# Kernel optimization log

Hardware: AMD Instinct MI355X
Metric: run time of the kernel (lower is better)

Reference implementation:

```python
import jax, jax.numpy as jnp
import numpy as np

H = 1024
S = 2048
B = 16

def setup_inputs() -> dict:
    key = jax.random.key(0)
    k1, k2, k3, k4, k5, k6 = jax.random.split(key, 6)
    hidden = jax.random.normal(k1, (1, B, H), dtype=jnp.float32)
    encoder_outputs = jax.random.normal(k2, (S, B, H), dtype=jnp.float32)
    seq_mask = jax.random.randint(k3, (B, S), 0, 2, dtype=jnp.int32)
    # nn.Linear(2H, H): weight [H, 2H], bias [H]
    lim1 = 1.0 / np.sqrt(2 * H)
    attn_w = jax.random.uniform(k4, (H, 2 * H), minval=-lim1, maxval=lim1, dtype=jnp.float32)
    attn_b = jax.random.uniform(k5, (H,), minval=-lim1, maxval=lim1, dtype=jnp.float32)
    # nn.Linear(H, 1, bias=False): weight [1, H]
    lim2 = 1.0 / np.sqrt(H)
    score_w = jax.random.uniform(k6, (1, H), minval=-lim2, maxval=lim2, dtype=jnp.float32)
    return {"hidden": hidden, "encoder_outputs": encoder_outputs, "seq_mask": seq_mask,
            "attn_w": attn_w, "attn_b": attn_b, "score_w": score_w}

def reference(hidden, encoder_outputs, seq_mask, attn_w, attn_b, score_w):
    # Faithful to: cat([hidden.repeat(S,1,1), encoder_outputs], -1) @ attn_w.T + attn_b
    # Split the concat-linear into two GEMMs (identical math, avoids the big concat).
    h = hidden.shape[-1]
    Wh = attn_w[:, :h]   # acts on repeated hidden
    We = attn_w[:, h:]   # acts on encoder outputs
    # hidden: [1,B,H] broadcasts over S; encoder_outputs: [S,B,H]
    pre = jnp.einsum('obh,kh->obk', hidden, Wh) + jnp.einsum('sbh,kh->sbk', encoder_outputs, We) + attn_b
    proj = jnp.tanh(pre)                               # [S,B,H]
    energies = jnp.einsum('sbh,oh->sbo', proj, score_w)[..., 0]  # [S,B]
    energies = energies.T                              # [B,S] (transpose(0,1) in original)
    energies = jnp.where(seq_mask.astype(bool), jnp.float32(-1e12), energies)
    attn = jax.nn.softmax(energies, axis=1)            # [B,S]
    return attn[:, None, :]                            # [B,1,S]
```

## Files before the change

### kernel.cpp

```cpp
#include <hip/hip_runtime.h>
#include <hip/hip_bf16.h>

#define HDIM 1024
#define SEQ 2048
#define BATCH 16
#define M_TOT (SEQ*BATCH)
#define NBLK 4
#define BM 256
#define BN 256
#define BKT 64
#define NT (HDIM/BKT)

typedef __attribute__((ext_vector_type(8))) short short8;
typedef __attribute__((ext_vector_type(4))) float f32x4;

typedef const void __attribute__((address_space(1))) gvoid_t;
typedef void __attribute__((address_space(3))) svoid_t;
#define GLD16(gp, lp) __builtin_amdgcn_global_load_lds((gvoid_t*)(gp), (svoid_t*)(lp), 16, 0, 0)
#define VMC(N) asm volatile("s_waitcnt vmcnt(" #N ")" ::: "memory")

static __device__ __forceinline__ unsigned short f2bf(float f) {
    unsigned int x = __float_as_uint(f);
    unsigned int r = (x + 0x7FFFu + ((x >> 16) & 1u)) >> 16;
    return (unsigned short)r;
}

__global__ __launch_bounds__(256) void qk_kernel(const float* __restrict__ hidden,
                                                 const float* __restrict__ attn_w,
                                                 const float* __restrict__ attn_b,
                                                 float* __restrict__ q) {
    int k = blockIdx.x;
    int tid = threadIdx.x;
    const float* w = attn_w + (size_t)k * (2 * HDIM);
    float p[BATCH];
#pragma unroll
    for (int b = 0; b < BATCH; b++) p[b] = 0.f;
    for (int h = tid; h < HDIM; h += 256) {
        float wv = w[h];
#pragma unroll
        for (int b = 0; b < BATCH; b++) p[b] += hidden[b * HDIM + h] * wv;
    }
#pragma unroll
    for (int b = 0; b < BATCH; b++) {
        for (int off = 32; off; off >>= 1) p[b] += __shfl_down(p[b], off);
    }
    __shared__ float red[4][BATCH];
    int lane = tid & 63, wid = tid >> 6;
    if (lane == 0) {
#pragma unroll
        for (int b = 0; b < BATCH; b++) red[wid][b] = p[b];
    }
    __syncthreads();
    if (tid < BATCH) {
        float s = red[0][tid] + red[1][tid] + red[2][tid] + red[3][tid] + attn_b[k];
        q[(size_t)tid * HDIM + k] = s;
    }
}

__global__ __launch_bounds__(256) void conv_kernel(const float* __restrict__ attn_w,
                                                   __hip_bfloat16* __restrict__ web) {
    size_t i0 = ((size_t)blockIdx.x * 256 + threadIdx.x) * 8;
    int n = (int)(i0 >> 10);
    int h = (int)(i0 & 1023);
    const float4* src = reinterpret_cast<const float4*>(attn_w + (size_t)n * (2 * HDIM) + HDIM + h);
    float4 a = src[0], b = src[1];
    union { unsigned short u[8]; short8 v; } cv;
    cv.u[0] = f2bf(a.x); cv.u[1] = f2bf(a.y); cv.u[2] = f2bf(a.z); cv.u[3] = f2bf(a.w);
    cv.u[4] = f2bf(b.x); cv.u[5] = f2bf(b.y); cv.u[6] = f2bf(b.z); cv.u[7] = f2bf(b.w);
    *reinterpret_cast<short8*>((unsigned short*)web + i0) = cv.v;
}

__global__ __launch_bounds__(256) void conv_enc(const float* __restrict__ src,
                                                __hip_bfloat16* __restrict__ dst) {
    size_t i0 = ((size_t)blockIdx.x * 256 + threadIdx.x) * 8;
    const float4* s = reinterpret_cast<const float4*>(src + i0);
    float4 a = s[0], b = s[1];
    union { unsigned short u[8]; short8 v; } cv;
    cv.u[0] = f2bf(a.x); cv.u[1] = f2bf(a.y); cv.u[2] = f2bf(a.z); cv.u[3] = f2bf(a.w);
    cv.u[4] = f2bf(b.x); cv.u[5] = f2bf(b.y); cv.u[6] = f2bf(b.z); cv.u[7] = f2bf(b.w);
    *reinterpret_cast<short8*>((unsigned short*)dst + i0) = cv.v;
}

__global__ __launch_bounds__(512, 2) void gemm8(const __hip_bfloat16* __restrict__ encb,
                                                const __hip_bfloat16* __restrict__ web,
                                                const float* __restrict__ qv,
                                                const float* __restrict__ score_w,
                                                float* __restrict__ part) {
    __shared__ __align__(16) char pool[131072];

    int tid = threadIdx.x;
    int lane = tid & 63;
    int wid = tid >> 6;
    int wr = wid >> 2;
    int wc = wid & 3;

    int bid = blockIdx.x;
    int lin = (bid & 7) * 64 + (bid >> 3);
    int bm = lin >> 2;
    int bn = lin & 3;
    int m0 = bm * BM, n0 = bn * BN;

    int srow = tid >> 3;
    int scolb = (((tid & 7) ^ ((tid >> 3) & 7)) << 4);
    const char* eb = (const char*)encb;
    const char* wb = (const char*)web;

    auto STG = [&](const char* g, int ldsoff) {
        GLD16(g + (size_t)srow * 2048 + scolb, pool + ldsoff + wid * 1024);
        GLD16(g + (size_t)(srow + 64) * 2048 + scolb, pool + ldsoff + 8192 + wid * 1024);
    };
    auto APTR = [&](int kt, int h) { return eb + ((size_t)(m0 + h * 128) * HDIM + kt * BKT) * 2; };
    auto BPTR = [&](int kt, int h) { return wb + ((size_t)(n0 + h * 128) * HDIM + kt * BKT) * 2; };
#define ALDS(par, h) ((par) * 32768 + (h) * 16384)
#define BLDS(par, h) (65536 + (par) * 32768 + (h) * 16384)

    int lq = lane & 15, lh = lane >> 4;
    int flip = (lane & 7) << 4;
    int pks0 = lq * 128 + ((lh * 16) ^ flip);
    int pks1 = lq * 128 + (((64 + lh * 16)) ^ flip);
    int aFB = wr * 16384;
    int bFB = 65536 + (wc >> 1) * 16384 + (wc & 1) * 8192;

    f32x4 acc[8][4];
#pragma unroll
    for (int i = 0; i < 8; i++)
#pragma unroll
        for (int j = 0; j < 4; j++) acc[i][j] = (f32x4)0.f;
    short8 br[4][2];

#define RD8(off) (*reinterpret_cast<const short8*>(pool + (off)))

#define PHASE(Q, PAR, STAGE_STMT, PRE_CLOSE)                                              \
    {                                                                                     \
        if ((Q) == 0) {                                                                   \
            _Pragma("unroll") for (int nj = 0; nj < 4; ++nj) {                            \
                br[nj][0] = RD8(bFB + (PAR) * 32768 + nj * 2048 + pks0);                  \
                br[nj][1] = RD8(bFB + (PAR) * 32768 + nj * 2048 + pks1);                  \
            }                                                                             \
        }                                                                                 \
        short8 a0k0 = RD8(aFB + (PAR) * 32768 + (2 * (Q)) * 2048 + pks0);                 \
        short8 a0k1 = RD8(aFB + (PAR) * 32768 + (2 * (Q)) * 2048 + pks1);                 \
        short8 a1k0 = RD8(aFB + (PAR) * 32768 + (2 * (Q) + 1) * 2048 + pks0);             \
        short8 a1k1 = RD8(aFB + (PAR) * 32768 + (2 * (Q) + 1) * 2048 + pks1);             \
        STAGE_STMT;                                                                       \
        __builtin_amdgcn_s_barrier();                                                     \
        __builtin_amdgcn_s_setprio(1);                                                    \
        _Pragma("unroll") for (int nj = 0; nj < 4; ++nj) {                                \
            acc[2 * (Q)][nj] = __builtin_amdgcn_mfma_f32_16x16x32_bf16(a0k0, br[nj][0], acc[2 * (Q)][nj], 0, 0, 0); \
            acc[2 * (Q)][nj] = __builtin_amdgcn_mfma_f32_16x16x32_bf16(a0k1, br[nj][1], acc[2 * (Q)][nj], 0, 0, 0); \
            acc[2 * (Q) + 1][nj] = __builtin_amdgcn_mfma_f32_16x16x32_bf16(a1k0, br[nj][0], acc[2 * (Q) + 1][nj], 0, 0, 0); \
            acc[2 * (Q) + 1][nj] = __builtin_amdgcn_mfma_f32_16x16x32_bf16(a1k1, br[nj][1], acc[2 * (Q) + 1][nj], 0, 0, 0); \
        }                                                                                 \
        __builtin_amdgcn_s_setprio(0);                                                    \
        PRE_CLOSE;                                                                        \
        __builtin_amdgcn_s_barrier();                                                     \
        __builtin_amdgcn_sched_barrier(0);                                                \
    }

    STG(BPTR(0, 0), BLDS(0, 0));
    STG(BPTR(0, 1), BLDS(0, 1));
    STG(APTR(0, 0), ALDS(0, 0));
    STG(APTR(0, 1), ALDS(0, 1));
    STG(BPTR(1, 0), BLDS(1, 0));
    STG(BPTR(1, 1), BLDS(1, 1));
    VMC(4);
    __builtin_amdgcn_s_barrier();
    __builtin_amdgcn_sched_barrier(0);

#pragma unroll 1
    for (int J = 0; J < 7; ++J) {
        int k1 = 2 * J + 1;
        PHASE(0, 0, STG(APTR(k1, 0), ALDS(1, 0)), );
        PHASE(1, 0, STG(APTR(k1, 1), ALDS(1, 1)), );
        PHASE(2, 0, STG(BPTR(k1 + 1, 0), BLDS(0, 0)), );
        PHASE(3, 0, STG(BPTR(k1 + 1, 1), BLDS(0, 1)), VMC(4));
        PHASE(0, 1, STG(APTR(k1 + 1, 0), ALDS(0, 0)), );
        PHASE(1, 1, STG(APTR(k1 + 1, 1), ALDS(0, 1)), );
        PHASE(2, 1, STG(BPTR(k1 + 2, 0), BLDS(1, 0)), );
        PHASE(3, 1, STG(BPTR(k1 + 2, 1), BLDS(1, 1)), VMC(4));
    }
    PHASE(0, 0, STG(APTR(15, 0), ALDS(1, 0)), );
    PHASE(1, 0, STG(APTR(15, 1), ALDS(1, 1)), );
    PHASE(2, 0, , );
    PHASE(3, 0, , VMC(0));
    PHASE(0, 1, , );
    PHASE(1, 1, , );
    PHASE(2, 1, , );
    PHASE(3, 1, , );

    float* q_lds = reinterpret_cast<float*>(pool);
    float* sc_lds = reinterpret_cast<float*>(pool + 16384);
    float* eng = reinterpret_cast<float*>(pool + 17408);
    {
        int qb = tid >> 5;
        int kl = (tid & 31) * 8;
        const float4* src = reinterpret_cast<const float4*>(qv + (size_t)qb * HDIM + n0 + kl);
        float4 v0 = src[0], v1 = src[1];
        *reinterpret_cast<float4*>(&q_lds[qb * 256 + kl]) = v0;
        *reinterpret_cast<float4*>(&q_lds[qb * 256 + kl + 4]) = v1;
        if (tid < BN) sc_lds[tid] = score_w[n0 + tid];
    }
    __syncthreads();

#pragma unroll
    for (int mi = 0; mi < 8; ++mi) {
#pragma unroll
        for (int r = 0; r < 4; ++r) {
            int b = lh * 4 + r;
            float s = 0.f;
#pragma unroll
            for (int nj = 0; nj < 4; ++nj) {
                int kl = wc * 64 + nj * 16 + lq;
                float v = acc[mi][nj][r] + q_lds[b * 256 + kl];
                float t = 1.f - 2.f / (__expf(2.f * v) + 1.f);
                s += sc_lds[kl] * t;
            }
            for (int off = 1; off < 16; off <<= 1) s += __shfl_xor(s, off);
            if (lq == 0) eng[wc * 256 + wr * 128 + mi * 16 + b] = s;
        }
    }
    __syncthreads();
    if (tid < BM) {
        float s = eng[tid] + eng[256 + tid] + eng[512 + tid] + eng[768 + tid];
        part[(size_t)bn * M_TOT + m0 + tid] = s;
    }
#undef PHASE
#undef RD8
#undef ALDS
#undef BLDS
}

__global__ __launch_bounds__(256) void softmax_kernel(const float* __restrict__ part,
                                                      const int* __restrict__ mask,
                                                      float* __restrict__ out) {
    int b = blockIdx.x;
    int tid = threadIdx.x;
    __shared__ float e_lds[SEQ];
    __shared__ float red[4], red2[4];
    int lane = tid & 63, wid = tid >> 6;
    float lmax = -3.4e38f;
    for (int it = 0; it < SEQ / 256; ++it) {
        int s = it * 256 + tid;
        size_t m = (size_t)s * BATCH + b;
        float e = 0.f;
#pragma unroll
        for (int c = 0; c < NBLK; c++) e += part[(size_t)c * M_TOT + m];
        if (mask[(size_t)b * SEQ + s]) e = -1e12f;
        e_lds[s] = e;
        lmax = fmaxf(lmax, e);
    }
    for (int off = 32; off; off >>= 1) lmax = fmaxf(lmax, __shfl_xor(lmax, off));
    if (lane == 0) red[wid] = lmax;
    __syncthreads();
    float gmax = fmaxf(fmaxf(red[0], red[1]), fmaxf(red[2], red[3]));
    float lsum = 0.f;
    for (int it = 0; it < SEQ / 256; ++it) {
        int s = it * 256 + tid;
        float p = __expf(e_lds[s] - gmax);
        e_lds[s] = p;
        lsum += p;
    }
    for (int off = 32; off; off >>= 1) lsum += __shfl_xor(lsum, off);
    if (lane == 0) red2[wid] = lsum;
    __syncthreads();
    float inv = 1.f / (red2[0] + red2[1] + red2[2] + red2[3]);
    for (int it = 0; it < SEQ / 256; ++it) {
        int s = it * 256 + tid;
        out[(size_t)b * SEQ + s] = e_lds[s] * inv;
    }
}

extern "C" void kernel_launch(void* const* d_in, const int* in_sizes, int n_in,
                              void* d_out, int out_size, void* d_ws, size_t ws_size,
                              hipStream_t stream) {
    const float* hidden   = (const float*)d_in[0];
    const float* enc      = (const float*)d_in[1];
    const int*   seq_mask = (const int*)d_in[2];
    const float* attn_w   = (const float*)d_in[3];
    const float* attn_b   = (const float*)d_in[4];
    const float* score_w  = (const float*)d_in[5];
    float* out = (float*)d_out;

    char* ws = (char*)d_ws;
    float* q = (float*)ws;
    __hip_bfloat16* web = (__hip_bfloat16*)(ws + 65536);
    float* part = (float*)(ws + 65536 + 2 * 1024 * 1024);
    __hip_bfloat16* encb = (__hip_bfloat16*)(ws + 65536 + 3 * 1024 * 1024);

    conv_enc<<<dim3((M_TOT * HDIM) / (8 * 256)), dim3(256), 0, stream>>>(enc, encb);
    conv_kernel<<<dim3((HDIM * HDIM) / (8 * 256)), dim3(256), 0, stream>>>(attn_w, web);
    qk_kernel<<<dim3(HDIM), dim3(256), 0, stream>>>(hidden, attn_w, attn_b, q);
    gemm8<<<dim3(NBLK * (M_TOT / BM)), dim3(512), 0, stream>>>(encb, web, q, score_w, part);
    softmax_kernel<<<dim3(BATCH), dim3(256), 0, stream>>>(part, seq_mask, out);
}
```

Before: 121.7 us.

## Fuse fp32-to-bf16 encoder conversion into GEMM A-tile loads via registers

```diff
diff --git a/kernel.cpp b/kernel.cpp
--- a/kernel.cpp
+++ b/kernel.cpp
@@ -18,6 +18,7 @@
 typedef void __attribute__((address_space(3))) svoid_t;
 #define GLD16(gp, lp) __builtin_amdgcn_global_load_lds((gvoid_t*)(gp), (svoid_t*)(lp), 16, 0, 0)
 #define VMC(N) asm volatile("s_waitcnt vmcnt(" #N ")" ::: "memory")
+#define LGKM0 asm volatile("s_waitcnt lgkmcnt(0)" ::: "memory")
 
 static __device__ __forceinline__ unsigned short f2bf(float f) {
     unsigned int x = __float_as_uint(f);
@@ -70,18 +71,7 @@
     *reinterpret_cast<short8*>((unsigned short*)web + i0) = cv.v;
 }
 
-__global__ __launch_bounds__(256) void conv_enc(const float* __restrict__ src,
-                                                __hip_bfloat16* __restrict__ dst) {
-    size_t i0 = ((size_t)blockIdx.x * 256 + threadIdx.x) * 8;
-    const float4* s = reinterpret_cast<const float4*>(src + i0);
-    float4 a = s[0], b = s[1];
-    union { unsigned short u[8]; short8 v; } cv;
-    cv.u[0] = f2bf(a.x); cv.u[1] = f2bf(a.y); cv.u[2] = f2bf(a.z); cv.u[3] = f2bf(a.w);
-    cv.u[4] = f2bf(b.x); cv.u[5] = f2bf(b.y); cv.u[6] = f2bf(b.z); cv.u[7] = f2bf(b.w);
-    *reinterpret_cast<short8*>((unsigned short*)dst + i0) = cv.v;
-}
-
-__global__ __launch_bounds__(512, 2) void gemm8(const __hip_bfloat16* __restrict__ encb,
+__global__ __launch_bounds__(512, 2) void gemm8(const float* __restrict__ enc,
                                                 const __hip_bfloat16* __restrict__ web,
                                                 const float* __restrict__ qv,
                                                 const float* __restrict__ score_w,
@@ -102,17 +92,43 @@
 
     int srow = tid >> 3;
     int scolb = (((tid & 7) ^ ((tid >> 3) & 7)) << 4);
-    const char* eb = (const char*)encb;
     const char* wb = (const char*)web;
 
     auto STG = [&](const char* g, int ldsoff) {
         GLD16(g + (size_t)srow * 2048 + scolb, pool + ldsoff + wid * 1024);
         GLD16(g + (size_t)(srow + 64) * 2048 + scolb, pool + ldsoff + 8192 + wid * 1024);
     };
-    auto APTR = [&](int kt, int h) { return eb + ((size_t)(m0 + h * 128) * HDIM + kt * BKT) * 2; };
     auto BPTR = [&](int kt, int h) { return wb + ((size_t)(n0 + h * 128) * HDIM + kt * BKT) * 2; };
 #define ALDS(par, h) ((par) * 32768 + (h) * 16384)
 #define BLDS(par, h) (65536 + (par) * 32768 + (h) * 16384)
+
+    int ar = tid >> 2;
+    int ac = (tid & 3) * 16;
+    int awc = ((tid & 3) * 32) ^ ((ar & 7) << 4);
+    float4 av_e[8], av_o[8];
+
+    auto ALD = [&](float4* d, int kt, int h) {
+        const float4* p = reinterpret_cast<const float4*>(enc + (size_t)(m0 + h * 128 + ar) * HDIM + kt * BKT + ac);
+        d[0] = p[0]; d[1] = p[1]; d[2] = p[2]; d[3] = p[3];
+    };
+    auto AWR = [&](float4* v, int par) {
+#pragma unroll
+        for (int h = 0; h < 2; ++h) {
+            const float4* s4 = v + h * 4;
+            union { __hip_bfloat162 b[4]; short8 s; } w0, w1;
+            w0.b[0] = __float22bfloat162_rn(make_float2(s4[0].x, s4[0].y));
+            w0.b[1] = __float22bfloat162_rn(make_float2(s4[0].z, s4[0].w));
+            w0.b[2] = __float22bfloat162_rn(make_float2(s4[1].x, s4[1].y));
+            w0.b[3] = __float22bfloat162_rn(make_float2(s4[1].z, s4[1].w));
+            w1.b[0] = __float22bfloat162_rn(make_float2(s4[2].x, s4[2].y));
+            w1.b[1] = __float22bfloat162_rn(make_float2(s4[2].z, s4[2].w));
+            w1.b[2] = __float22bfloat162_rn(make_float2(s4[3].x, s4[3].y));
+            w1.b[3] = __float22bfloat162_rn(make_float2(s4[3].z, s4[3].w));
+            char* base = pool + par * 32768 + h * 16384 + ar * 128;
+            *reinterpret_cast<short8*>(base + awc) = w0.s;
+            *reinterpret_cast<short8*>(base + (awc ^ 16)) = w1.s;
+        }
+    };
 
     int lq = lane & 15, lh = lane >> 4;
     int flip = (lane & 7) << 4;
@@ -157,32 +173,37 @@
         __builtin_amdgcn_sched_barrier(0);                                                \
     }
 
+    ALD(av_o, 0, 0);
+    ALD(av_o + 4, 0, 1);
     STG(BPTR(0, 0), BLDS(0, 0));
     STG(BPTR(0, 1), BLDS(0, 1));
-    STG(APTR(0, 0), ALDS(0, 0));
-    STG(APTR(0, 1), ALDS(0, 1));
+    VMC(4);
+    AWR(av_o, 0);
+    ALD(av_o, 1, 0);
+    ALD(av_o + 4, 1, 1);
     STG(BPTR(1, 0), BLDS(1, 0));
     STG(BPTR(1, 1), BLDS(1, 1));
-    VMC(4);
+    VMC(12);
+    LGKM0;
     __builtin_amdgcn_s_barrier();
     __builtin_amdgcn_sched_barrier(0);
 
 #pragma unroll 1
     for (int J = 0; J < 7; ++J) {
-        int k1 = 2 * J + 1;
-        PHASE(0, 0, STG(APTR(k1, 0), ALDS(1, 0)), );
-        PHASE(1, 0, STG(APTR(k1, 1), ALDS(1, 1)), );
-        PHASE(2, 0, STG(BPTR(k1 + 1, 0), BLDS(0, 0)), );
-        PHASE(3, 0, STG(BPTR(k1 + 1, 1), BLDS(0, 1)), VMC(4));
-        PHASE(0, 1, STG(APTR(k1 + 1, 0), ALDS(0, 0)), );
-        PHASE(1, 1, STG(APTR(k1 + 1, 1), ALDS(0, 1)), );
-        PHASE(2, 1, STG(BPTR(k1 + 2, 0), BLDS(1, 0)), );
-        PHASE(3, 1, STG(BPTR(k1 + 2, 1), BLDS(1, 1)), VMC(4));
-    }
-    PHASE(0, 0, STG(APTR(15, 0), ALDS(1, 0)), );
-    PHASE(1, 0, STG(APTR(15, 1), ALDS(1, 1)), );
-    PHASE(2, 0, , );
-    PHASE(3, 0, , VMC(0));
+        int ke = 2 * J + 2, ko = 2 * J + 3;
+        PHASE(0, 0, ALD(av_e, ke, 0), );
+        PHASE(1, 0, ALD(av_e + 4, ke, 1), );
+        PHASE(2, 0, { VMC(8); AWR(av_o, 1); }, LGKM0);
+        PHASE(3, 0, { STG(BPTR(ke, 0), BLDS(0, 0)); STG(BPTR(ke, 1), BLDS(0, 1)); }, );
+        PHASE(0, 1, ALD(av_o, ko, 0), );
+        PHASE(1, 1, ALD(av_o + 4, ko, 1), );
+        PHASE(2, 1, { VMC(8); AWR(av_e, 0); }, LGKM0);
+        PHASE(3, 1, { STG(BPTR(ko, 0), BLDS(1, 0)); STG(BPTR(ko, 1), BLDS(1, 1)); }, );
+    }
+    PHASE(0, 0, , );
+    PHASE(1, 0, , );
+    PHASE(2, 0, { VMC(0); AWR(av_o, 1); }, LGKM0);
+    PHASE(3, 0, , );
     PHASE(0, 1, , );
     PHASE(1, 1, , );
     PHASE(2, 1, , );
@@ -285,11 +306,9 @@
     float* q = (float*)ws;
     __hip_bfloat16* web = (__hip_bfloat16*)(ws + 65536);
     float* part = (float*)(ws + 65536 + 2 * 1024 * 1024);
-    __hip_bfloat16* encb = (__hip_bfloat16*)(ws + 65536 + 3 * 1024 * 1024);
-
-    conv_enc<<<dim3((M_TOT * HDIM) / (8 * 256)), dim3(256), 0, stream>>>(enc, encb);
+
     conv_kernel<<<dim3((HDIM * HDIM) / (8 * 256)), dim3(256), 0, stream>>>(attn_w, web);
     qk_kernel<<<dim3(HDIM), dim3(256), 0, stream>>>(hidden, attn_w, attn_b, q);
-    gemm8<<<dim3(NBLK * (M_TOT / BM)), dim3(512), 0, stream>>>(encb, web, q, score_w, part);
+    gemm8<<<dim3(NBLK * (M_TOT / BM)), dim3(512), 0, stream>>>(enc, web, q, score_w, part);
     softmax_kernel<<<dim3(BATCH), dim3(256), 0, stream>>>(part, seq_mask, out);
 }
```

Result: slower. 226.8 us (+86.4%).

## Fuse encoder fp32-to-bf16 conversion into GEMM A-tile loads and merge prep kernels

Applied to the files above, without the earlier changes.

```diff
diff --git a/kernel.cpp b/kernel.cpp
--- a/kernel.cpp
+++ b/kernel.cpp
@@ -5,9 +5,9 @@
 #define SEQ 2048
 #define BATCH 16
 #define M_TOT (SEQ*BATCH)
-#define NBLK 4
+#define NBLK 8
 #define BM 256
-#define BN 256
+#define BN 128
 #define BKT 64
 #define NT (HDIM/BKT)
 
@@ -18,6 +18,7 @@
 typedef void __attribute__((address_space(3))) svoid_t;
 #define GLD16(gp, lp) __builtin_amdgcn_global_load_lds((gvoid_t*)(gp), (svoid_t*)(lp), 16, 0, 0)
 #define VMC(N) asm volatile("s_waitcnt vmcnt(" #N ")" ::: "memory")
+#define LGKM0 asm volatile("s_waitcnt lgkmcnt(0)" ::: "memory")
 
 static __device__ __forceinline__ unsigned short f2bf(float f) {
     unsigned int x = __float_as_uint(f);
@@ -25,11 +26,25 @@
     return (unsigned short)r;
 }
 
-__global__ __launch_bounds__(256) void qk_kernel(const float* __restrict__ hidden,
-                                                 const float* __restrict__ attn_w,
-                                                 const float* __restrict__ attn_b,
-                                                 float* __restrict__ q) {
-    int k = blockIdx.x;
+__global__ __launch_bounds__(256) void prep_kernel(const float* __restrict__ hidden,
+                                                   const float* __restrict__ attn_w,
+                                                   const float* __restrict__ attn_b,
+                                                   float* __restrict__ q,
+                                                   __hip_bfloat16* __restrict__ web) {
+    int bid = blockIdx.x;
+    if (bid < 512) {
+        size_t i0 = ((size_t)bid * 256 + threadIdx.x) * 8;
+        int n = (int)(i0 >> 10);
+        int h = (int)(i0 & 1023);
+        const float4* src = reinterpret_cast<const float4*>(attn_w + (size_t)n * (2 * HDIM) + HDIM + h);
+        float4 a = src[0], b = src[1];
+        union { unsigned short u[8]; short8 v; } cv;
+        cv.u[0] = f2bf(a.x); cv.u[1] = f2bf(a.y); cv.u[2] = f2bf(a.z); cv.u[3] = f2bf(a.w);
+        cv.u[4] = f2bf(b.x); cv.u[5] = f2bf(b.y); cv.u[6] = f2bf(b.z); cv.u[7] = f2bf(b.w);
+        *reinterpret_cast<short8*>((unsigned short*)web + i0) = cv.v;
+        return;
+    }
+    int k = bid - 512;
     int tid = threadIdx.x;
     const float* w = attn_w + (size_t)k * (2 * HDIM);
     float p[BATCH];
@@ -57,153 +72,154 @@
     }
 }
 
-__global__ __launch_bounds__(256) void conv_kernel(const float* __restrict__ attn_w,
-                                                   __hip_bfloat16* __restrict__ web) {
-    size_t i0 = ((size_t)blockIdx.x * 256 + threadIdx.x) * 8;
-    int n = (int)(i0 >> 10);
-    int h = (int)(i0 & 1023);
-    const float4* src = reinterpret_cast<const float4*>(attn_w + (size_t)n * (2 * HDIM) + HDIM + h);
-    float4 a = src[0], b = src[1];
-    union { unsigned short u[8]; short8 v; } cv;
-    cv.u[0] = f2bf(a.x); cv.u[1] = f2bf(a.y); cv.u[2] = f2bf(a.z); cv.u[3] = f2bf(a.w);
-    cv.u[4] = f2bf(b.x); cv.u[5] = f2bf(b.y); cv.u[6] = f2bf(b.z); cv.u[7] = f2bf(b.w);
-    *reinterpret_cast<short8*>((unsigned short*)web + i0) = cv.v;
-}
-
-__global__ __launch_bounds__(256) void conv_enc(const float* __restrict__ src,
-                                                __hip_bfloat16* __restrict__ dst) {
-    size_t i0 = ((size_t)blockIdx.x * 256 + threadIdx.x) * 8;
-    const float4* s = reinterpret_cast<const float4*>(src + i0);
-    float4 a = s[0], b = s[1];
-    union { unsigned short u[8]; short8 v; } cv;
-    cv.u[0] = f2bf(a.x); cv.u[1] = f2bf(a.y); cv.u[2] = f2bf(a.z); cv.u[3] = f2bf(a.w);
-    cv.u[4] = f2bf(b.x); cv.u[5] = f2bf(b.y); cv.u[6] = f2bf(b.z); cv.u[7] = f2bf(b.w);
-    *reinterpret_cast<short8*>((unsigned short*)dst + i0) = cv.v;
-}
-
-__global__ __launch_bounds__(512, 2) void gemm8(const __hip_bfloat16* __restrict__ encb,
+__global__ __launch_bounds__(512, 2) void gemm8(const float* __restrict__ enc,
                                                 const __hip_bfloat16* __restrict__ web,
                                                 const float* __restrict__ qv,
                                                 const float* __restrict__ score_w,
                                                 float* __restrict__ part) {
-    __shared__ __align__(16) char pool[131072];
+    __shared__ __align__(16) char pool[98304];
 
     int tid = threadIdx.x;
     int lane = tid & 63;
     int wid = tid >> 6;
-    int wr = wid >> 2;
-    int wc = wid & 3;
+    int wr = wid >> 1;
+    int wc = wid & 1;
 
     int bid = blockIdx.x;
-    int lin = (bid & 7) * 64 + (bid >> 3);
-    int bm = lin >> 2;
-    int bn = lin & 3;
+    int lin = (bid & 7) * 128 + (bid >> 3);
+    int bm = lin >> 3;
+    int bn = lin & 7;
     int m0 = bm * BM, n0 = bn * BN;
 
-    int srow = tid >> 3;
-    int scolb = (((tid & 7) ^ ((tid >> 3) & 7)) << 4);
-    const char* eb = (const char*)encb;
     const char* wb = (const char*)web;
-
-    auto STG = [&](const char* g, int ldsoff) {
-        GLD16(g + (size_t)srow * 2048 + scolb, pool + ldsoff + wid * 1024);
-        GLD16(g + (size_t)(srow + 64) * 2048 + scolb, pool + ldsoff + 8192 + wid * 1024);
+    int brow = wid * 8 + (lane >> 3);
+    int bsegb = (((lane & 7) ^ ((lane >> 3) & 7)) << 4);
+    auto BSTG = [&](int kt, int p) {
+        const char* g0 = wb + ((size_t)(n0 + brow) * HDIM + kt * BKT) * 2 + bsegb;
+        GLD16(g0, pool + 65536 + p * 16384 + wid * 1024);
+        const char* g1 = wb + ((size_t)(n0 + 64 + brow) * HDIM + kt * BKT) * 2 + bsegb;
+        GLD16(g1, pool + 65536 + p * 16384 + 8192 + wid * 1024);
     };
-    auto APTR = [&](int kt, int h) { return eb + ((size_t)(m0 + h * 128) * HDIM + kt * BKT) * 2; };
-    auto BPTR = [&](int kt, int h) { return wb + ((size_t)(n0 + h * 128) * HDIM + kt * BKT) * 2; };
-#define ALDS(par, h) ((par) * 32768 + (h) * 16384)
-#define BLDS(par, h) (65536 + (par) * 32768 + (h) * 16384)
+
+    int arow = tid >> 1;
+    int ah = tid & 1;
+    const float* abase = enc + (size_t)(m0 + arow) * HDIM + ah * 32;
+    float4 av[8];
+    auto ALD = [&](int kt) {
+        const float4* p = reinterpret_cast<const float4*>(abase + kt * BKT);
+#pragma unroll
+        for (int i = 0; i < 8; i++) av[i] = p[i];
+    };
+    int ar7 = arow & 7;
+    auto AWR = [&](int p) {
+        char* base = pool + p * 32768 + arow * 128;
+#pragma unroll
+        for (int w = 0; w < 4; w++) {
+            union { __hip_bfloat162 b[4]; short8 s; } u;
+            u.b[0] = __float22bfloat162_rn(make_float2(av[2 * w].x, av[2 * w].y));
+            u.b[1] = __float22bfloat162_rn(make_float2(av[2 * w].z, av[2 * w].w));
+            u.b[2] = __float22bfloat162_rn(make_float2(av[2 * w + 1].x, av[2 * w + 1].y));
+            u.b[3] = __float22bfloat162_rn(make_float2(av[2 * w + 1].z, av[2 * w + 1].w));
+            *reinterpret_cast<short8*>(base + (((ah * 4 + w) ^ ar7) << 4)) = u.s;
+        }
+    };
 
     int lq = lane & 15, lh = lane >> 4;
-    int flip = (lane & 7) << 4;
-    int pks0 = lq * 128 + ((lh * 16) ^ flip);
-    int pks1 = lq * 128 + (((64 + lh * 16)) ^ flip);
-    int aFB = wr * 16384;
-    int bFB = 65536 + (wc >> 1) * 16384 + (wc & 1) * 8192;
-
-    f32x4 acc[8][4];
-#pragma unroll
-    for (int i = 0; i < 8; i++)
+    int s0 = ((lh ^ (lq & 7)) << 4);
+    int s1 = (((4 + lh) ^ (lq & 7)) << 4);
+    int aRB = (wr * 64 + lq) * 128;
+    int bRB = 65536 + (wc * 64 + lq) * 128;
+
+    f32x4 acc[4][4];
+#pragma unroll
+    for (int i = 0; i < 4; i++)
 #pragma unroll
         for (int j = 0; j < 4; j++) acc[i][j] = (f32x4)0.f;
     short8 br[4][2];
 
 #define RD8(off) (*reinterpret_cast<const short8*>(pool + (off)))
 
-#define PHASE(Q, PAR, STAGE_STMT, PRE_CLOSE)                                              \
+#define PH1(PAR, T)                                                                       \
     {                                                                                     \
-        if ((Q) == 0) {                                                                   \
-            _Pragma("unroll") for (int nj = 0; nj < 4; ++nj) {                            \
-                br[nj][0] = RD8(bFB + (PAR) * 32768 + nj * 2048 + pks0);                  \
-                br[nj][1] = RD8(bFB + (PAR) * 32768 + nj * 2048 + pks1);                  \
-            }                                                                             \
+        _Pragma("unroll") for (int nj = 0; nj < 4; ++nj) {                                \
+            br[nj][0] = RD8(bRB + (PAR) * 16384 + nj * 2048 + s0);                        \
+            br[nj][1] = RD8(bRB + (PAR) * 16384 + nj * 2048 + s1);                        \
         }                                                                                 \
-        short8 a0k0 = RD8(aFB + (PAR) * 32768 + (2 * (Q)) * 2048 + pks0);                 \
-        short8 a0k1 = RD8(aFB + (PAR) * 32768 + (2 * (Q)) * 2048 + pks1);                 \
-        short8 a1k0 = RD8(aFB + (PAR) * 32768 + (2 * (Q) + 1) * 2048 + pks0);             \
-        short8 a1k1 = RD8(aFB + (PAR) * 32768 + (2 * (Q) + 1) * 2048 + pks1);             \
-        STAGE_STMT;                                                                       \
+        short8 a00 = RD8(aRB + (PAR) * 32768 + 0 * 2048 + s0);                            \
+        short8 a01 = RD8(aRB + (PAR) * 32768 + 0 * 2048 + s1);                            \
+        short8 a10 = RD8(aRB + (PAR) * 32768 + 1 * 2048 + s0);                            \
+        short8 a11 = RD8(aRB + (PAR) * 32768 + 1 * 2048 + s1);                            \
+        if ((T) < 15) ALD((T) + 1);                                                       \
         __builtin_amdgcn_s_barrier();                                                     \
         __builtin_amdgcn_s_setprio(1);                                                    \
         _Pragma("unroll") for (int nj = 0; nj < 4; ++nj) {                                \
-            acc[2 * (Q)][nj] = __builtin_amdgcn_mfma_f32_16x16x32_bf16(a0k0, br[nj][0], acc[2 * (Q)][nj], 0, 0, 0); \
-            acc[2 * (Q)][nj] = __builtin_amdgcn_mfma_f32_16x16x32_bf16(a0k1, br[nj][1], acc[2 * (Q)][nj], 0, 0, 0); \
-            acc[2 * (Q) + 1][nj] = __builtin_amdgcn_mfma_f32_16x16x32_bf16(a1k0, br[nj][0], acc[2 * (Q) + 1][nj], 0, 0, 0); \
-            acc[2 * (Q) + 1][nj] = __builtin_amdgcn_mfma_f32_16x16x32_bf16(a1k1, br[nj][1], acc[2 * (Q) + 1][nj], 0, 0, 0); \
+            acc[0][nj] = __builtin_amdgcn_mfma_f32_16x16x32_bf16(a00, br[nj][0], acc[0][nj], 0, 0, 0); \
+            acc[0][nj] = __builtin_amdgcn_mfma_f32_16x16x32_bf16(a01, br[nj][1], acc[0][nj], 0, 0, 0); \
+            acc[1][nj] = __builtin_amdgcn_mfma_f32_16x16x32_bf16(a10, br[nj][0], acc[1][nj], 0, 0, 0); \
+            acc[1][nj] = __builtin_amdgcn_mfma_f32_16x16x32_bf16(a11, br[nj][1], acc[1][nj], 0, 0, 0); \
         }                                                                                 \
         __builtin_amdgcn_s_setprio(0);                                                    \
-        PRE_CLOSE;                                                                        \
         __builtin_amdgcn_s_barrier();                                                     \
         __builtin_amdgcn_sched_barrier(0);                                                \
     }
 
-    STG(BPTR(0, 0), BLDS(0, 0));
-    STG(BPTR(0, 1), BLDS(0, 1));
-    STG(APTR(0, 0), ALDS(0, 0));
-    STG(APTR(0, 1), ALDS(0, 1));
-    STG(BPTR(1, 0), BLDS(1, 0));
-    STG(BPTR(1, 1), BLDS(1, 1));
-    VMC(4);
+#define PH2(PAR, T)                                                                       \
+    {                                                                                     \
+        short8 a00 = RD8(aRB + (PAR) * 32768 + 2 * 2048 + s0);                            \
+        short8 a01 = RD8(aRB + (PAR) * 32768 + 2 * 2048 + s1);                            \
+        short8 a10 = RD8(aRB + (PAR) * 32768 + 3 * 2048 + s0);                            \
+        short8 a11 = RD8(aRB + (PAR) * 32768 + 3 * 2048 + s1);                            \
+        VMC(0);                                                                           \
+        if ((T) < 15) AWR((PAR) ^ 1);                                                     \
+        if ((T) < 14) BSTG((T) + 2, (PAR));                                               \
+        LGKM0;                                                                            \
+        __builtin_amdgcn_sched_barrier(0);                                                \
+        __builtin_amdgcn_s_barrier();                                                     \
+        __builtin_amdgcn_s_setprio(1);                                                    \
+        _Pragma("unroll") for (int nj = 0; nj < 4; ++nj) {                                \
+            acc[2][nj] = __builtin_amdgcn_mfma_f32_16x16x32_bf16(a00, br[nj][0], acc[2][nj], 0, 0, 0); \
+            acc[2][nj] = __builtin_amdgcn_mfma_f32_16x16x32_bf16(a01, br[nj][1], acc[2][nj], 0, 0, 0); \
+            acc[3][nj] = __builtin_amdgcn_mfma_f32_16x16x32_bf16(a10, br[nj][0], acc[3][nj], 0, 0, 0); \
+            acc[3][nj] = __builtin_amdgcn_mfma_f32_16x16x32_bf16(a11, br[nj][1], acc[3][nj], 0, 0, 0); \
+        }                                                                                 \
+        __builtin_amdgcn_s_setprio(0);                                                    \
+        __builtin_amdgcn_s_barrier();                                                     \
+        __builtin_amdgcn_sched_barrier(0);                                                \
+    }
+
+    ALD(0);
+    VMC(0);
+    AWR(0);
+    BSTG(0, 0);
+    BSTG(1, 1);
+    VMC(2);
+    LGKM0;
     __builtin_amdgcn_s_barrier();
     __builtin_amdgcn_sched_barrier(0);
 
 #pragma unroll 1
-    for (int J = 0; J < 7; ++J) {
-        int k1 = 2 * J + 1;
-        PHASE(0, 0, STG(APTR(k1, 0), ALDS(1, 0)), );
-        PHASE(1, 0, STG(APTR(k1, 1), ALDS(1, 1)), );
-        PHASE(2, 0, STG(BPTR(k1 + 1, 0), BLDS(0, 0)), );
-        PHASE(3, 0, STG(BPTR(k1 + 1, 1), BLDS(0, 1)), VMC(4));
-        PHASE(0, 1, STG(APTR(k1 + 1, 0), ALDS(0, 0)), );
-        PHASE(1, 1, STG(APTR(k1 + 1, 1), ALDS(0, 1)), );
-        PHASE(2, 1, STG(BPTR(k1 + 2, 0), BLDS(1, 0)), );
-        PHASE(3, 1, STG(BPTR(k1 + 2, 1), BLDS(1, 1)), VMC(4));
-    }
-    PHASE(0, 0, STG(APTR(15, 0), ALDS(1, 0)), );
-    PHASE(1, 0, STG(APTR(15, 1), ALDS(1, 1)), );
-    PHASE(2, 0, , );
-    PHASE(3, 0, , VMC(0));
-    PHASE(0, 1, , );
-    PHASE(1, 1, , );
-    PHASE(2, 1, , );
-    PHASE(3, 1, , );
+    for (int tp = 0; tp < 8; ++tp) {
+        int t0 = 2 * tp, t1 = 2 * tp + 1;
+        PH1(0, t0);
+        PH2(0, t0);
+        PH1(1, t1);
+        PH2(1, t1);
+    }
 
     float* q_lds = reinterpret_cast<float*>(pool);
-    float* sc_lds = reinterpret_cast<float*>(pool + 16384);
-    float* eng = reinterpret_cast<float*>(pool + 17408);
+    float* sc_lds = reinterpret_cast<float*>(pool + 8192);
+    float* eng = reinterpret_cast<float*>(pool + 8704);
     {
         int qb = tid >> 5;
-        int kl = (tid & 31) * 8;
-        const float4* src = reinterpret_cast<const float4*>(qv + (size_t)qb * HDIM + n0 + kl);
-        float4 v0 = src[0], v1 = src[1];
-        *reinterpret_cast<float4*>(&q_lds[qb * 256 + kl]) = v0;
-        *reinterpret_cast<float4*>(&q_lds[qb * 256 + kl + 4]) = v1;
+        int kl = (tid & 31) * 4;
+        *reinterpret_cast<float4*>(&q_lds[qb * 128 + kl]) =
+            *reinterpret_cast<const float4*>(qv + (size_t)qb * HDIM + n0 + kl);
         if (tid < BN) sc_lds[tid] = score_w[n0 + tid];
     }
     __syncthreads();
 
 #pragma unroll
-    for (int mi = 0; mi < 8; ++mi) {
+    for (int mi = 0; mi < 4; ++mi) {
 #pragma unroll
         for (int r = 0; r < 4; ++r) {
             int b = lh * 4 + r;
@@ -211,23 +227,19 @@
 #pragma unroll
             for (int nj = 0; nj < 4; ++nj) {
                 int kl = wc * 64 + nj * 16 + lq;
-                float v = acc[mi][nj][r] + q_lds[b * 256 + kl];
+                float v = acc[mi][nj][r] + q_lds[b * 128 + kl];
                 float t = 1.f - 2.f / (__expf(2.f * v) + 1.f);
                 s += sc_lds[kl] * t;
             }
             for (int off = 1; off < 16; off <<= 1) s += __shfl_xor(s, off);
-            if (lq == 0) eng[wc * 256 + wr * 128 + mi * 16 + b] = s;
+            if (lq == 0) eng[wc * 256 + wr * 64 + mi * 16 + b] = s;
         }
     }
     __syncthreads();
-    if (tid < BM) {
-        float s = eng[tid] + eng[256 + tid] + eng[512 + tid] + eng[768 + tid];
-        part[(size_t)bn * M_TOT + m0 + tid] = s;
-    }
-#undef PHASE
+    if (tid < BM) part[(size_t)bn * M_TOT + m0 + tid] = eng[tid] + eng[256 + tid];
+#undef PH1
+#undef PH2
 #undef RD8
-#undef ALDS
-#undef BLDS
 }
 
 __global__ __launch_bounds__(256) void softmax_kernel(const float* __restrict__ part,
@@ -285,11 +297,8 @@
     float* q = (float*)ws;
     __hip_bfloat16* web = (__hip_bfloat16*)(ws + 65536);
     float* part = (float*)(ws + 65536 + 2 * 1024 * 1024);
-    __hip_bfloat16* encb = (__hip_bfloat16*)(ws + 65536 + 3 * 1024 * 1024);
-
-    conv_enc<<<dim3((M_TOT * HDIM) / (8 * 256)), dim3(256), 0, stream>>>(enc, encb);
-    conv_kernel<<<dim3((HDIM * HDIM) / (8 * 256)), dim3(256), 0, stream>>>(attn_w, web);
-    qk_kernel<<<dim3(HDIM), dim3(256), 0, stream>>>(hidden, attn_w, attn_b, q);
-    gemm8<<<dim3(NBLK * (M_TOT / BM)), dim3(512), 0, stream>>>(encb, web, q, score_w, part);
+
+    prep_kernel<<<dim3(512 + HDIM), dim3(256), 0, stream>>>(hidden, attn_w, attn_b, q, web);
+    gemm8<<<dim3(NBLK * (M_TOT / BM)), dim3(512), 0, stream>>>(enc, web, q, score_w, part);
     softmax_kernel<<<dim3(BATCH), dim3(256), 0, stream>>>(part, seq_mask, out);
 }
```

Result: slower. 216.7 us (+78.1%).
